# Kernel optimization log

Hardware: AMD Instinct MI355X
Metric: run time of the kernel (lower is better)

Reference implementation:

```python
import jax, jax.numpy as jnp
import numpy as np

EPS = 1e-3  # tf.keras.layers.BatchNormalization default epsilon


def setup_inputs() -> dict:
    key = jax.random.key(0)
    k1, k2 = jax.random.split(key)
    B, N, F = 16, 8192, 256
    voxel_features = jax.random.normal(k1, (B, N, F), dtype=jnp.float32)
    num_valid_voxels = jax.random.randint(k2, (B,), 0, N, dtype=jnp.int32)
    gamma = jnp.ones((F,), dtype=jnp.float32)
    beta = jnp.zeros((F,), dtype=jnp.float32)
    return {
        "voxel_features": voxel_features,
        "num_valid_voxels": num_valid_voxels,
        "gamma": gamma,
        "beta": beta,
    }


def reference(voxel_features, num_valid_voxels, gamma, beta):
    # voxel_features: [B, N, F]; num_valid_voxels: [B]
    B, N, F = voxel_features.shape
    # mask[b, n] = n < num_valid_voxels[b]
    mask = (jnp.arange(N, dtype=jnp.int32)[None, :] < num_valid_voxels[:, None])
    maskf = mask.astype(voxel_features.dtype)[:, :, None]  # [B, N, 1]
    count = jnp.maximum(jnp.sum(num_valid_voxels).astype(voxel_features.dtype), 1.0)
    xm = voxel_features * maskf
    # Batch statistics over valid voxels only (per-feature), biased variance as BN uses
    mean = jnp.sum(xm, axis=(0, 1)) / count                      # [F]
    var = jnp.sum((voxel_features - mean) ** 2 * maskf, axis=(0, 1)) / count  # [F]
    inv_std = jax.lax.rsqrt(var + EPS)
    normed = (voxel_features - mean) * inv_std * gamma + beta
    # Padding positions are zeroed (the original pads unpadded outputs with zeros)
    return normed * maskf
```

## Files before the change

kernel.cpp:

```cpp
#include <hip/hip_runtime.h>

#define Bdim 16
#define Ndim 8192
#define Fdim 256
#define ROWS (Bdim * Ndim)
#define CHUNKS_PER_ROW (Fdim / 4)
#define TOTAL_CHUNKS (ROWS * CHUNKS_PER_ROW)

#define REDUCE_BLOCKS 512
#define NORM_BLOCKS 8192
#define EPS 1e-3f


__global__ __launch_bounds__(512) void init_kernel(float* __restrict__ ws) {
    ws[threadIdx.x] = 0.0f;
}

__global__ __launch_bounds__(256) void reduce_kernel(
    const float* __restrict__ x, const int* __restrict__ nv,
    float* __restrict__ ws)
{
    __shared__ float lds_s[4][Fdim];
    __shared__ float lds_q[4][Fdim];
    __shared__ int s_nv[Bdim];
    const int tid = threadIdx.x;
    if (tid < Bdim) s_nv[tid] = nv[tid];
    __syncthreads();

    const int c = tid & 63;
    const int r = tid >> 6;
    const int f0 = c * 4;

    float sum0 = 0.f, sum1 = 0.f, sum2 = 0.f, sum3 = 0.f;
    float sq0 = 0.f, sq1 = 0.f, sq2 = 0.f, sq3 = 0.f;

    const int rows_per_block = ROWS / REDUCE_BLOCKS;
    const int row0 = blockIdx.x * rows_per_block;
    for (int i = r; i < rows_per_block; i += 4) {
        const int row = row0 + i;
        const int b = row >> 13;
        const int n = row & (Ndim - 1);
        if (n < s_nv[b]) {
            const float4 v = *((const float4*)(x + (size_t)row * Fdim) + c);
            sum0 += v.x; sq0 += v.x * v.x;
            sum1 += v.y; sq1 += v.y * v.y;
            sum2 += v.z; sq2 += v.z * v.z;
            sum3 += v.w; sq3 += v.w * v.w;
        }
    }

    lds_s[r][f0 + 0] = sum0; lds_s[r][f0 + 1] = sum1;
    lds_s[r][f0 + 2] = sum2; lds_s[r][f0 + 3] = sum3;
    lds_q[r][f0 + 0] = sq0;  lds_q[r][f0 + 1] = sq1;
    lds_q[r][f0 + 2] = sq2;  lds_q[r][f0 + 3] = sq3;
    __syncthreads();

    float ts = 0.0f, tq = 0.0f;
    #pragma unroll
    for (int rr = 0; rr < 4; rr++) { ts += lds_s[rr][tid]; tq += lds_q[rr][tid]; }
    unsafeAtomicAdd(&ws[tid], ts);
    unsafeAtomicAdd(&ws[Fdim + tid], tq);
}

__global__ __launch_bounds__(256) void finalize_kernel(
    const int* __restrict__ nv, const float* __restrict__ gamma,
    const float* __restrict__ beta, float* __restrict__ ws)
{
    __shared__ float s_count;
    const int tid = threadIdx.x;
    if (tid == 0) {
        int cnt = 0;
        for (int i = 0; i < Bdim; i++) cnt += nv[i];
        s_count = fmaxf((float)cnt, 1.0f);
    }
    __syncthreads();
    const float inv_count = 1.0f / s_count;
    const float mean = ws[tid] * inv_count;
    float var = ws[Fdim + tid] * inv_count - mean * mean;
    var = fmaxf(var, 0.0f);
    const float inv_std = rsqrtf(var + EPS);
    const float s = inv_std * gamma[tid];
    ws[2 * Fdim + tid] = s;
    ws[3 * Fdim + tid] = beta[tid] - mean * s;
}

__global__ __launch_bounds__(256) void norm_kernel(
    const float* __restrict__ x, const int* __restrict__ nv,
    const float* __restrict__ ws, float* __restrict__ out)
{
    __shared__ int s_nv[Bdim];
    const int tid = threadIdx.x;
    if (tid < Bdim) s_nv[tid] = nv[tid];

    const int c = tid & 63;
    const float4 sc = ((const float4*)(ws + 2 * Fdim))[c];
    const float4 bi = ((const float4*)(ws + 3 * Fdim))[c];
    __syncthreads();

    const int base = blockIdx.x * 256 + tid;
    const int stride = NORM_BLOCKS * 256;
    #pragma unroll
    for (int it = 0; it < TOTAL_CHUNKS / (NORM_BLOCKS * 256); it++) {
        const int idx = base + it * stride;
        const int row = idx >> 6;
        const int b = row >> 13;
        const int n = row & (Ndim - 1);
        float4* po = (float4*)out + idx;
        if (n < s_nv[b]) {
            const float4 v = ((const float4*)x)[idx];
            float4 o;
            o.x = fmaf(v.x, sc.x, bi.x);
            o.y = fmaf(v.y, sc.y, bi.y);
            o.z = fmaf(v.z, sc.z, bi.z);
            o.w = fmaf(v.w, sc.w, bi.w);
            *po = o;
        } else {
            *po = make_float4(0.f, 0.f, 0.f, 0.f);
        }
    }
}

extern "C" void kernel_launch(void* const* d_in, const int* in_sizes, int n_in,
                              void* d_out, int out_size, void* d_ws, size_t ws_size,
                              hipStream_t stream) {
    const float* x     = (const float*)d_in[0];
    const int*   nv    = (const int*)d_in[1];
    const float* gamma = (const float*)d_in[2];
    const float* beta  = (const float*)d_in[3];
    float* out = (float*)d_out;
    float* ws  = (float*)d_ws;

    init_kernel<<<1, 512, 0, stream>>>(ws);
    reduce_kernel<<<REDUCE_BLOCKS, 256, 0, stream>>>(x, nv, ws);
    finalize_kernel<<<1, 256, 0, stream>>>(nv, gamma, beta, ws);
    norm_kernel<<<NORM_BLOCKS, 256, 0, stream>>>(x, nv, ws, out);
}
```

Baseline: 255.9 us.

## Fold finalize into norm kernel, batch-aligned reduce with unrolled loads, nontemporal stores

Removes the separate finalize launch by having every norm block recompute the per-feature scale and bias into LDS from the accumulated sums. The reduce kernel now assigns 64 blocks per batch and computes the valid row count once, so it loops only over valid rows with a 4-way unrolled load body instead of testing every row. Output stores use nontemporal hints to limit cache pollution. Each of the 8192 norm blocks now redundantly performs a small reduction over nv plus an rsqrt, which adds a little per-block work.

```diff
diff --git a/kernel.cpp b/kernel.cpp
--- a/kernel.cpp
+++ b/kernel.cpp
@@ -3,13 +3,16 @@
 #define Bdim 16
 #define Ndim 8192
 #define Fdim 256
-#define ROWS (Bdim * Ndim)
-#define CHUNKS_PER_ROW (Fdim / 4)
-#define TOTAL_CHUNKS (ROWS * CHUNKS_PER_ROW)
+#define EPS 1e-3f
 
-#define REDUCE_BLOCKS 512
+#define RED_BLOCKS_PER_BATCH 64
+#define RED_BLOCKS (Bdim * RED_BLOCKS_PER_BATCH)
+#define RED_ROWS_PER_BLOCK (Ndim / RED_BLOCKS_PER_BATCH)
+
 #define NORM_BLOCKS 8192
-#define EPS 1e-3f
+#define TOTAL_CHUNKS (Bdim * Ndim * (Fdim / 4))
+
+typedef float fx4 __attribute__((ext_vector_type(4)));
 
 
 __global__ __launch_bounds__(512) void init_kernel(float* __restrict__ ws) {
@@ -22,37 +25,43 @@
 {
     __shared__ float lds_s[4][Fdim];
     __shared__ float lds_q[4][Fdim];
-    __shared__ int s_nv[Bdim];
     const int tid = threadIdx.x;
-    if (tid < Bdim) s_nv[tid] = nv[tid];
-    __syncthreads();
+    const int b   = blockIdx.x >> 6;
+    const int rb0 = (blockIdx.x & 63) * RED_ROWS_PER_BLOCK;
+    const int nvb = nv[b];
+    int valid = nvb - rb0;
+    valid = valid < 0 ? 0 : (valid > RED_ROWS_PER_BLOCK ? RED_ROWS_PER_BLOCK : valid);
 
     const int c = tid & 63;
     const int r = tid >> 6;
-    const int f0 = c * 4;
+    const fx4* xb = (const fx4*)(x + ((size_t)b * Ndim + rb0) * Fdim) + c;
 
-    float sum0 = 0.f, sum1 = 0.f, sum2 = 0.f, sum3 = 0.f;
-    float sq0 = 0.f, sq1 = 0.f, sq2 = 0.f, sq3 = 0.f;
+    float s0=0.f,s1=0.f,s2=0.f,s3=0.f, q0=0.f,q1=0.f,q2=0.f,q3=0.f;
 
-    const int rows_per_block = ROWS / REDUCE_BLOCKS;
-    const int row0 = blockIdx.x * rows_per_block;
-    for (int i = r; i < rows_per_block; i += 4) {
-        const int row = row0 + i;
-        const int b = row >> 13;
-        const int n = row & (Ndim - 1);
-        if (n < s_nv[b]) {
-            const float4 v = *((const float4*)(x + (size_t)row * Fdim) + c);
-            sum0 += v.x; sq0 += v.x * v.x;
-            sum1 += v.y; sq1 += v.y * v.y;
-            sum2 += v.z; sq2 += v.z * v.z;
-            sum3 += v.w; sq3 += v.w * v.w;
-        }
+    int i = r;
+    for (; i + 12 < valid; i += 16) {
+        const fx4 v0 = xb[(size_t)(i     ) * 64];
+        const fx4 v1 = xb[(size_t)(i +  4) * 64];
+        const fx4 v2 = xb[(size_t)(i +  8) * 64];
+        const fx4 v3 = xb[(size_t)(i + 12) * 64];
+        s0 += v0.x; q0 += v0.x*v0.x;  s1 += v0.y; q1 += v0.y*v0.y;
+        s2 += v0.z; q2 += v0.z*v0.z;  s3 += v0.w; q3 += v0.w*v0.w;
+        s0 += v1.x; q0 += v1.x*v1.x;  s1 += v1.y; q1 += v1.y*v1.y;
+        s2 += v1.z; q2 += v1.z*v1.z;  s3 += v1.w; q3 += v1.w*v1.w;
+        s0 += v2.x; q0 += v2.x*v2.x;  s1 += v2.y; q1 += v2.y*v2.y;
+        s2 += v2.z; q2 += v2.z*v2.z;  s3 += v2.w; q3 += v2.w*v2.w;
+        s0 += v3.x; q0 += v3.x*v3.x;  s1 += v3.y; q1 += v3.y*v3.y;
+        s2 += v3.z; q2 += v3.z*v3.z;  s3 += v3.w; q3 += v3.w*v3.w;
+    }
+    for (; i < valid; i += 4) {
+        const fx4 v = xb[(size_t)i * 64];
+        s0 += v.x; q0 += v.x*v.x;  s1 += v.y; q1 += v.y*v.y;
+        s2 += v.z; q2 += v.z*v.z;  s3 += v.w; q3 += v.w*v.w;
     }
 
-    lds_s[r][f0 + 0] = sum0; lds_s[r][f0 + 1] = sum1;
-    lds_s[r][f0 + 2] = sum2; lds_s[r][f0 + 3] = sum3;
-    lds_q[r][f0 + 0] = sq0;  lds_q[r][f0 + 1] = sq1;
-    lds_q[r][f0 + 2] = sq2;  lds_q[r][f0 + 3] = sq3;
+    const int f0 = c * 4;
+    lds_s[r][f0+0]=s0; lds_s[r][f0+1]=s1; lds_s[r][f0+2]=s2; lds_s[r][f0+3]=s3;
+    lds_q[r][f0+0]=q0; lds_q[r][f0+1]=q1; lds_q[r][f0+2]=q2; lds_q[r][f0+3]=q3;
     __syncthreads();
 
     float ts = 0.0f, tq = 0.0f;
@@ -62,40 +71,33 @@
     unsafeAtomicAdd(&ws[Fdim + tid], tq);
 }
 
-__global__ __launch_bounds__(256) void finalize_kernel(
-    const int* __restrict__ nv, const float* __restrict__ gamma,
-    const float* __restrict__ beta, float* __restrict__ ws)
-{
-    __shared__ float s_count;
-    const int tid = threadIdx.x;
-    if (tid == 0) {
-        int cnt = 0;
-        for (int i = 0; i < Bdim; i++) cnt += nv[i];
-        s_count = fmaxf((float)cnt, 1.0f);
-    }
-    __syncthreads();
-    const float inv_count = 1.0f / s_count;
-    const float mean = ws[tid] * inv_count;
-    float var = ws[Fdim + tid] * inv_count - mean * mean;
-    var = fmaxf(var, 0.0f);
-    const float inv_std = rsqrtf(var + EPS);
-    const float s = inv_std * gamma[tid];
-    ws[2 * Fdim + tid] = s;
-    ws[3 * Fdim + tid] = beta[tid] - mean * s;
-}
-
 __global__ __launch_bounds__(256) void norm_kernel(
     const float* __restrict__ x, const int* __restrict__ nv,
+    const float* __restrict__ gamma, const float* __restrict__ beta,
     const float* __restrict__ ws, float* __restrict__ out)
 {
+    __shared__ float s_sc[Fdim], s_bi[Fdim];
     __shared__ int s_nv[Bdim];
     const int tid = threadIdx.x;
     if (tid < Bdim) s_nv[tid] = nv[tid];
+    __syncthreads();
+    {
+        int cnt = 0;
+        #pragma unroll
+        for (int i = 0; i < Bdim; i++) cnt += s_nv[i];
+        const float inv_count = 1.0f / fmaxf((float)cnt, 1.0f);
+        const float mean = ws[tid] * inv_count;
+        float var = fmaf(ws[Fdim + tid], inv_count, -mean * mean);
+        var = fmaxf(var, 0.0f);
+        const float s = rsqrtf(var + EPS) * gamma[tid];
+        s_sc[tid] = s;
+        s_bi[tid] = fmaf(-mean, s, beta[tid]);
+    }
+    __syncthreads();
 
     const int c = tid & 63;
-    const float4 sc = ((const float4*)(ws + 2 * Fdim))[c];
-    const float4 bi = ((const float4*)(ws + 3 * Fdim))[c];
-    __syncthreads();
+    const fx4 sc = ((const fx4*)s_sc)[c];
+    const fx4 bi = ((const fx4*)s_bi)[c];
 
     const int base = blockIdx.x * 256 + tid;
     const int stride = NORM_BLOCKS * 256;
@@ -105,17 +107,18 @@
         const int row = idx >> 6;
         const int b = row >> 13;
         const int n = row & (Ndim - 1);
-        float4* po = (float4*)out + idx;
+        fx4* po = (fx4*)out + idx;
         if (n < s_nv[b]) {
-            const float4 v = ((const float4*)x)[idx];
-            float4 o;
+            const fx4 v = ((const fx4*)x)[idx];
+            fx4 o;
             o.x = fmaf(v.x, sc.x, bi.x);
             o.y = fmaf(v.y, sc.y, bi.y);
             o.z = fmaf(v.z, sc.z, bi.z);
             o.w = fmaf(v.w, sc.w, bi.w);
-            *po = o;
+            __builtin_nontemporal_store(o, po);
         } else {
-            *po = make_float4(0.f, 0.f, 0.f, 0.f);
+            const fx4 z = {0.f, 0.f, 0.f, 0.f};
+            __builtin_nontemporal_store(z, po);
         }
     }
 }
@@ -131,7 +134,6 @@
     float* ws  = (float*)d_ws;
 
     init_kernel<<<1, 512, 0, stream>>>(ws);
-    reduce_kernel<<<REDUCE_BLOCKS, 256, 0, stream>>>(x, nv, ws);
-    finalize_kernel<<<1, 256, 0, stream>>>(nv, gamma, beta, ws);
-    norm_kernel<<<NORM_BLOCKS, 256, 0, stream>>>(x, nv, ws, out);
+    reduce_kernel<<<RED_BLOCKS, 256, 0, stream>>>(x, nv, ws);
+    norm_kernel<<<NORM_BLOCKS, 256, 0, stream>>>(x, nv, gamma, beta, ws, out);
 }
```

New measurement: 235.0 us. 8.2% less time.
